# Performance work log

Measured on AMD Instinct MI355X. Metric: run time of the kernel, lower is better.

The kernel has to match this reference:

```python
import jax, jax.numpy as jnp
import numpy as np

B, S, Lc = 128, 128, 20          # batch, words per sentence, chars per word
AB, E = 100, 64                  # char alphabet, char embedding dim
Hc, H, OUT = 256, 512, 50        # char hidden, word hidden, n tags
PAD = 0                          # padding idx for words and chars


def _cell_params(key, din, h):
    k1, k2, k3, k4 = jax.random.split(key, 4)
    return (jax.random.normal(k1, (4 * h, din)) * 0.05,
            jax.random.normal(k2, (4 * h, h)) * 0.05,
            jax.random.normal(k3, (4 * h,)) * 0.05,
            jax.random.normal(k4, (4 * h,)) * 0.05)


def setup_inputs() -> dict:
    key = jax.random.key(0)
    ks = jax.random.split(key, 12)
    x = jax.random.randint(ks[0], (B, S, Lc), 0, AB)
    emb = jax.random.normal(ks[1], (AB, E)) * 0.05
    emb = emb.at[PAD].set(0.0)  # nn.Embedding padding_idx row is zero
    cW_ih, cW_hh, cb_ih, cb_hh = _cell_params(ks[2], E, Hc)
    fW_ih, fW_hh, fb_ih, fb_hh = _cell_params(ks[3], Hc, H)
    bW_ih, bW_hh, bb_ih, bb_hh = _cell_params(ks[4], Hc, H)
    W1 = jax.random.normal(ks[5], (256, 2 * H)) * 0.05
    b1 = jax.random.normal(ks[6], (256,)) * 0.05
    W2 = jax.random.normal(ks[7], (256, 256)) * 0.05
    b2 = jax.random.normal(ks[8], (256,)) * 0.05
    W3 = jax.random.normal(ks[9], (OUT, 256)) * 0.05
    b3 = jax.random.normal(ks[10], (OUT,)) * 0.05
    return dict(x=x, emb=emb,
                cW_ih=cW_ih, cW_hh=cW_hh, cb_ih=cb_ih, cb_hh=cb_hh,
                fW_ih=fW_ih, fW_hh=fW_hh, fb_ih=fb_ih, fb_hh=fb_hh,
                bW_ih=bW_ih, bW_hh=bW_hh, bb_ih=bb_ih, bb_hh=bb_hh,
                W1=W1, b1=b1, W2=W2, b2=b2, W3=W3, b3=b3)


def _lstm_cell(x_t, h, c, W_ih, W_hh, b_ih, b_hh):
    # PyTorch LSTMCell: gates ordered i, f, g, o
    g = x_t @ W_ih.T + b_ih + h @ W_hh.T + b_hh
    i, f, gg, o = jnp.split(g, 4, axis=-1)
    c = jax.nn.sigmoid(f) * c + jax.nn.sigmoid(i) * jnp.tanh(gg)
    h = jax.nn.sigmoid(o) * jnp.tanh(c)
    return h, c


def _char_acceptor(e_seq, lengths, W_ih, W_hh, b_ih, b_hh, hsize):
    # e_seq: [N, T, E]; returns last non-padded hidden state per row: [N, hsize]
    N, T, _ = e_seq.shape
    h0 = jnp.zeros((N, hsize), e_seq.dtype)

    def step(carry, inp):
        h, c, last = carry
        x_t, t = inp
        h, c = _lstm_cell(x_t, h, c, W_ih, W_hh, b_ih, b_hh)
        last = jnp.where((lengths > t)[:, None], h, last)
        return (h, c, last), None

    xs = (jnp.swapaxes(e_seq, 0, 1), jnp.arange(T))
    (_, _, last), _ = jax.lax.scan(step, (h0, h0, h0), xs)
    return last


def _lstm_transduce(seq_tbd, W_ih, W_hh, b_ih, b_hh, hsize):
    # seq_tbd: [T, B, D] -> all hidden states [T, B, hsize]
    Tb = seq_tbd.shape[1]
    h0 = jnp.zeros((Tb, hsize), seq_tbd.dtype)

    def step(carry, x_t):
        h, c = carry
        h, c = _lstm_cell(x_t, h, c, W_ih, W_hh, b_ih, b_hh)
        return (h, c), h

    _, hs = jax.lax.scan(step, (h0, h0), seq_tbd)
    return hs


def reference(x, emb,
              cW_ih, cW_hh, cb_ih, cb_hh,
              fW_ih, fW_hh, fb_ih, fb_hh,
              bW_ih, bW_hh, bb_ih, bb_hh,
              W1, b1, W2, b2, W3, b3):
    Bx, Sx, Lx = x.shape
    xf = x.reshape(Bx * Sx, Lx)                       # all words flattened
    e = emb[xf]                                       # [B*S, Lc, E]
    lengths = (xf != PAD).sum(axis=1)
    char_out = _char_acceptor(e, lengths, cW_ih, cW_hh, cb_ih, cb_hh, Hc)
    word_seq = char_out.reshape(Bx, Sx, Hc)           # [B, S, Hc]

    seq_tbd = jnp.swapaxes(word_seq, 0, 1)            # [S, B, Hc]
    hs_f = _lstm_transduce(seq_tbd, fW_ih, fW_hh, fb_ih, fb_hh, H)
    hs_b = _lstm_transduce(seq_tbd[::-1], bW_ih, bW_hh, bb_ih, bb_hh, H)[::-1]
    hs = jnp.concatenate([hs_f, hs_b], axis=-1)       # [S, B, 2H]
    hs = jnp.swapaxes(hs, 0, 1)                       # [B, S, 2H]

    h1 = jax.nn.relu(hs @ W1.T + b1)
    h2 = jax.nn.relu(h1 @ W2.T + b2)
    logits = h2 @ W3.T + b3                           # [B, S, OUT]
    return jax.nn.log_softmax(logits, axis=2)
```

## Files before the change

### kernel.cpp

```cpp
#include <hip/hip_runtime.h>
#include <hip/hip_bf16.h>
#include <math.h>

typedef __hip_bfloat16 bf16;
typedef __attribute__((ext_vector_type(8))) short bf16x8;
typedef __attribute__((ext_vector_type(4))) float f32x4;
typedef long i64t;

#define NW   16384
#define LC   20
#define EDIM 64
#define HC   256
#define HW   512
#define SEQ  128
#define NOUT 50
#define FPAD 16

#define LOG2E 1.4426950408889634f
__device__ __forceinline__ float fex2(float x) {
  float r; asm("v_exp_f32 %0, %1" : "=v"(r) : "v"(x)); return r;
}
__device__ __forceinline__ float frcp(float x) {
  float r; asm("v_rcp_f32 %0, %1" : "=v"(r) : "v"(x)); return r;
}
__device__ __forceinline__ float flog2(float x) {
  float r; asm("v_log_f32 %0, %1" : "=v"(r) : "v"(x)); return r;
}
__device__ __forceinline__ float fsig(float x) { return frcp(1.f + fex2(-LOG2E * x)); }
__device__ __forceinline__ float ftanh(float x) {
  return 1.f - 2.f * frcp(1.f + fex2(2.f * LOG2E * x));
}

__device__ __forceinline__ unsigned short f2bu(float f) {
  bf16 h = __float2bfloat16(f);
  return *reinterpret_cast<unsigned short*>(&h);
}
__device__ __forceinline__ bf16x8 ld8(const unsigned short* p) {
  return *reinterpret_cast<const bf16x8*>(p);
}
__device__ __forceinline__ float fp8_to_f32(unsigned int b) {
  float r; asm("v_cvt_f32_fp8 %0, %1" : "=v"(r) : "v"(b)); return r;
}
__device__ __forceinline__ i64t ld8x(const unsigned char* p, bool f) {
  i64t r;
  if (f) asm volatile("global_load_dwordx2 %0, %1, off sc0" : "=v"(r) : "v"(p));
  else   asm volatile("global_load_dwordx2 %0, %1, off sc0 sc1" : "=v"(r) : "v"(p));
  return r;
}
__device__ __forceinline__ void st8x(unsigned char* p, i64t v, bool f) {
  if (f) asm volatile("global_store_dwordx2 %0, %1, off sc0" :: "v"(p), "v"(v) : "memory");
  else   asm volatile("global_store_dwordx2 %0, %1, off sc0 sc1" :: "v"(p), "v"(v) : "memory");
}
__device__ __forceinline__ int ldflagx(const int* p, bool f) {
  int r;
  if (f) asm volatile("global_load_dword %0, %1, off sc0" : "=v"(r) : "v"(p));
  else   asm volatile("global_load_dword %0, %1, off sc0 sc1" : "=v"(r) : "v"(p));
  return r;
}
__device__ __forceinline__ void stflagx(int* p, int v, bool f) {
  if (f) asm volatile("global_store_dword %0, %1, off sc0" :: "v"(p), "v"(v) : "memory");
  else   asm volatile("global_store_dword %0, %1, off sc0 sc1" :: "v"(p), "v"(v) : "memory");
}
#define MFMA(a, b, c)  __builtin_amdgcn_mfma_f32_16x16x32_bf16(a, b, c, 0, 0, 0)
#define MFMA8(a, b, c) __builtin_amdgcn_mfma_f32_16x16x32_fp8_fp8(a, b, c, 0, 0, 0)

__global__ __launch_bounds__(512, 1) void char_lstm(
    const int* __restrict__ x, const unsigned char* __restrict__ emb8,
    const unsigned char* __restrict__ Wc8, const float* __restrict__ bcT,
    unsigned short* __restrict__ lastT, const int* __restrict__ len) {
  __shared__ unsigned char Hs8[2][64][264];
  __shared__ _Float16 Cs[256][66];
  __shared__ int lenS[64];
  const int tid = threadIdx.x;
  const int w = tid >> 6, l = tid & 63;
  const int l16 = l & 15, lk8 = (l >> 4) * 8, q = l >> 4;
  const int w0 = blockIdx.x * 64;
  if (tid < 64) lenS[tid] = len[w0 + tid];

  for (int t = 0; t < LC; ++t) {
    const int cur = t & 1, nxt = cur ^ 1;
    int xi[4];
#pragma unroll
    for (int wh = 0; wh < 4; ++wh) xi[wh] = x[(w0 + wh * 16 + l16) * LC + t];
#pragma unroll
    for (int c = 0; c < 2; ++c) {
      const int chg = w * 2 + c;
      const int cc0 = chg * 64;
      f32x4 acc[4][4] = {};
#pragma unroll
      for (int kk = 0; kk < 2; ++kk) {
        const int k = kk * 32 + lk8;
        const unsigned char* wp = Wc8 + (size_t)(cc0 + l16) * 320 + k;
        i64t bv8[4];
#pragma unroll
        for (int g = 0; g < 4; ++g)
          bv8[g] = *reinterpret_cast<const i64t*>(wp + g * 16 * 320);
#pragma unroll
        for (int wh = 0; wh < 4; ++wh) {
          i64t a8 = *reinterpret_cast<const i64t*>(emb8 + (size_t)xi[wh] * 64 + k);
#pragma unroll
          for (int g = 0; g < 4; ++g) acc[wh][g] = MFMA8(bv8[g], a8, acc[wh][g]);
        }
      }
      if (t > 0) {
#pragma unroll
        for (int kk = 2; kk < 10; ++kk) {
          const int k = kk * 32 + lk8;
          const unsigned char* wp = Wc8 + (size_t)(cc0 + l16) * 320 + k;
          i64t bv8[4];
#pragma unroll
          for (int g = 0; g < 4; ++g)
            bv8[g] = *reinterpret_cast<const i64t*>(wp + g * 16 * 320);
#pragma unroll
          for (int wh = 0; wh < 4; ++wh) {
            i64t a8 = *reinterpret_cast<const i64t*>(&Hs8[cur][wh * 16 + l16][k - 64]);
#pragma unroll
            for (int g = 0; g < 4; ++g) acc[wh][g] = MFMA8(bv8[g], a8, acc[wh][g]);
          }
        }
      }
      float4 bb4[4];
#pragma unroll
      for (int e = 0; e < 4; ++e)
        bb4[e] = *reinterpret_cast<const float4*>(bcT + (chg * 16 + q * 4 + e) * 4);
      const int uoff = chg * 16 + q * 4;
#pragma unroll
      for (int wh = 0; wh < 4; ++wh) {
        const int wd = wh * 16 + l16;
        float hv[4];
#pragma unroll
        for (int e = 0; e < 4; ++e) {
          const int ug = chg * 16 + q * 4 + e;
          const float gi = acc[wh][0][e] + bb4[e].x;
          const float gf = acc[wh][1][e] + bb4[e].y;
          const float gg = acc[wh][2][e] + bb4[e].z;
          const float go = acc[wh][3][e] + bb4[e].w;
          const float cprev = t ? (float)Cs[ug][wd] : 0.f;
          const float ccv = fsig(gf) * cprev + fsig(gi) * ftanh(gg);
          Cs[ug][wd] = (_Float16)ccv;
          hv[e] = fsig(go) * ftanh(ccv);
        }
        const int d0 = __builtin_amdgcn_cvt_pk_fp8_f32(hv[0], hv[1], 0, false);
        const int d1 = __builtin_amdgcn_cvt_pk_fp8_f32(hv[2], hv[3], 0, false);
        const unsigned int pk = (unsigned int)(d0 & 0xFFFF) |
                                ((unsigned int)(d1 & 0xFFFF) << 16);
        *reinterpret_cast<unsigned int*>(&Hs8[nxt][wd][uoff]) = pk;
      }
    }
    __syncthreads();
    {
      const int wd = tid >> 3, sub = tid & 7;
      const int myl = lenS[wd];
      if (myl == t + 1 || (myl == 0 && t == 0)) {
        const int n = w0 + wd;
        const int lrow = ((n & 127) * 128 + (n >> 7)) * HC;
        if (myl == 0) {
          bf16x8 z = {};
#pragma unroll
          for (int j = 0; j < 4; ++j)
            *reinterpret_cast<bf16x8*>(lastT + lrow + sub * 32 + j * 8) = z;
        } else {
#pragma unroll
          for (int j = 0; j < 4; ++j) {
            unsigned int v0 = *reinterpret_cast<unsigned int*>(
                &Hs8[nxt][wd][sub * 32 + j * 8]);
            unsigned int v1 = *reinterpret_cast<unsigned int*>(
                &Hs8[nxt][wd][sub * 32 + j * 8 + 4]);
            union { unsigned short s[8]; bf16x8 v; } o;
#pragma unroll
            for (int b = 0; b < 4; ++b) {
              o.s[b]     = f2bu(fp8_to_f32((v0 >> (8 * b)) & 0xFF));
              o.s[4 + b] = f2bu(fp8_to_f32((v1 >> (8 * b)) & 0xFF));
            }
            *reinterpret_cast<bf16x8*>(lastT + lrow + sub * 32 + j * 8) = o.v;
          }
        }
      }
    }
  }
}

__global__ __launch_bounds__(512, 1) void word_lstm(
    const unsigned short* __restrict__ lastT,
    const unsigned short* __restrict__ W16,
    const unsigned short* __restrict__ W16b,
    const unsigned char* __restrict__ W8f,
    const unsigned char* __restrict__ W8b,
    const float* __restrict__ bfi, const float* __restrict__ bbi,
    unsigned char* __restrict__ hbL8,
    unsigned short* __restrict__ hsW,
    int* __restrict__ aflag) {
  const int bx = blockIdx.x;
  if ((bx & 7) > 1) return;
  __shared__ unsigned short Wlds16[64 * 256];
  __shared__ unsigned char  Wlds8[64 * 512];
  __shared__ unsigned short ht[128][24];
  __shared__ unsigned char  ht8[128][24];
  __shared__ int fastS;
  const int tid = threadIdx.x;
  const int w = tid >> 6, l = tid & 63;
  const int l16 = l & 15, lk8 = (l >> 4) * 8, q = l >> 4;
  const int dir = bx & 7;
  const int nb = bx >> 3;
  const int c0 = nb * 64;
  const unsigned short* Wx = dir ? W16b : W16;
  const unsigned char*  Wh = dir ? W8b : W8f;
  const float* bias = dir ? bbi : bfi;
  int* negcnt = aflag + (size_t)2 * SEQ * 32 * FPAD;
  if (tid == 0) {
    const int xcc = __builtin_amdgcn_s_getreg(20 | (31 << 11)) & 7;
    int* xc = negcnt + 16 + dir * 8 + xcc;
    __hip_atomic_fetch_add(xc, 1, __ATOMIC_RELAXED, __HIP_MEMORY_SCOPE_AGENT);
    __hip_atomic_fetch_add(negcnt, 1, __ATOMIC_RELAXED, __HIP_MEMORY_SCOPE_AGENT);
    while (__hip_atomic_load(negcnt, __ATOMIC_RELAXED, __HIP_MEMORY_SCOPE_AGENT) < 64)
      __builtin_amdgcn_s_sleep(2);
    fastS = (__hip_atomic_load(xc, __ATOMIC_RELAXED, __HIP_MEMORY_SCOPE_AGENT) == 32);
  }
  for (int ci = tid; ci < 64 * 32; ci += 512) {
    const int col = ci >> 5, kc = (ci & 31) * 8;
    const int kcs = kc ^ ((col & 15) * 8);
    *reinterpret_cast<bf16x8*>(&Wlds16[col * 256 + kcs]) =
        ld8(Wx + (size_t)(c0 + col) * 256 + kc);
  }
  for (int ci = tid; ci < 64 * 64; ci += 512) {
    const int col = ci >> 6, kb = (ci & 63) * 8;
    const int kbs = kb ^ ((col & 15) * 8);
    *reinterpret_cast<i64t*>(&Wlds8[col * 512 + kbs]) =
        *reinterpret_cast<const i64t*>(Wh + (size_t)(c0 + col) * 512 + kb);
  }
  const float b0 = bias[c0 + 0 * 16 + l16];
  const float b1 = bias[c0 + 1 * 16 + l16];
  const float b2 = bias[c0 + 2 * 16 + l16];
  const float b3 = bias[c0 + 3 * 16 + l16];
  const int ksw = l16 * 8;
  float cst[4];
#pragma unroll
  for (int i = 0; i < 4; ++i) cst[i] = 0.f;
  __syncthreads();
  const bool fast = (fastS != 0);
  const int bt = w * 16 + l16;

  for (int t = 0; t < SEQ; ++t) {
    const int cur = t & 1;
    const int pos = dir ? (SEQ - 1 - t) : t;
    f32x4 acc[4] = {};
#pragma unroll
    for (int kk = 0; kk < 8; ++kk) {
      const int k = kk * 32 + lk8;
      bf16x8 a0 = ld8(lastT + ((size_t)pos * 128 + bt) * HC + k);
      const int ks = k ^ ksw;
#pragma unroll
      for (int nn = 0; nn < 4; ++nn) {
        bf16x8 bv = ld8(&Wlds16[(l16 + nn * 16) * 256 + ks]);
        acc[nn] = MFMA(a0, bv, acc[nn]);
      }
    }
    if (t > 0) {
      if (w == 0) {
        const int* fp = aflag + (size_t)(dir * SEQ + (t - 1)) * 32 * FPAD;
        for (;;) {
          int v = 1;
          if (l < 32) v = ldflagx(fp + l * FPAD, fast);
          if (__ballot(v != 0) == ~0ull) break;
          __builtin_amdgcn_s_sleep(1);
        }
      }
      __syncthreads();
      i64t af8[16];
      const unsigned char* hp =
          hbL8 + (size_t)(((cur ^ 1) * 2 + dir) * 32) * 128 * 16;
#pragma unroll
      for (int kk = 0; kk < 16; ++kk) {
        const int u = kk * 32 + lk8;
        const int nbs = u >> 4, ul = u & 15;
        af8[kk] = ld8x(hp + ((size_t)nbs * 128 + bt) * 16 + ul, fast);
      }
      asm volatile("s_waitcnt vmcnt(0)" ::: "memory");
      __builtin_amdgcn_sched_barrier(0);
#pragma unroll
      for (int kk = 0; kk < 16; ++kk) {
        const int ks8 = (kk * 32 + lk8) ^ ksw;
#pragma unroll
        for (int nn = 0; nn < 4; ++nn) {
          i64t w8 = *reinterpret_cast<const i64t*>(
              &Wlds8[(l16 + nn * 16) * 512 + ks8]);
          acc[nn] = MFMA8(af8[kk], w8, acc[nn]);
        }
      }
    }
    float hvf[4];
    int bats[4];
#pragma unroll
    for (int e = 0; e < 4; ++e) {
      const float gi = acc[0][e] + b0;
      const float gf = acc[1][e] + b1;
      const float gg = acc[2][e] + b2;
      const float go = acc[3][e] + b3;
      const float ccv = fsig(gf) * cst[e] + fsig(gi) * ftanh(gg);
      cst[e] = ccv;
      const float hv = fsig(go) * ftanh(ccv);
      const int bat = w * 16 + q * 4 + e;
      ht[bat][l16] = f2bu(hv);
      hvf[e] = hv; bats[e] = bat;
    }
    {
      const int d0 = __builtin_amdgcn_cvt_pk_fp8_f32(hvf[0], hvf[1], 0, false);
      const int d1 = __builtin_amdgcn_cvt_pk_fp8_f32(hvf[2], hvf[3], 0, false);
      ht8[bats[0]][l16] = (unsigned char)(d0 & 255);
      ht8[bats[1]][l16] = (unsigned char)((d0 >> 8) & 255);
      ht8[bats[2]][l16] = (unsigned char)(d1 & 255);
      ht8[bats[3]][l16] = (unsigned char)((d1 >> 8) & 255);
    }
    __syncthreads();
    if (tid < 256) {
      const int ub = tid >> 1, uh = tid & 1;
      i64t hv8 = *reinterpret_cast<const i64t*>(&ht8[ub][uh * 8]);
      st8x(hbL8 + (size_t)((cur * 2 + dir) * 32 + nb) * 128 * 16
               + ub * 16 + uh * 8, hv8, fast);
    }
    if (t < SEQ - 1) {
      asm volatile("s_waitcnt vmcnt(0)" ::: "memory");
      __syncthreads();
      if (tid == 0)
        stflagx(aflag + ((size_t)(dir * SEQ + t) * 32 + nb) * FPAD, 1, fast);
    }
    if (tid < 256) {
      const int ub = tid >> 1, uh = tid & 1;
      bf16x8 hv = ld8(&ht[ub][uh * 8]);
      *reinterpret_cast<bf16x8*>(
          hsW + (((size_t)(dir * 32 + nb) * 128 + pos) * 128 + ub) * 16 + uh * 8) = hv;
    }
  }
}

__global__ __launch_bounds__(256) void mlp1_gemm(
    const unsigned short* __restrict__ hsW, const unsigned short* __restrict__ W1b,
    const float* __restrict__ bias, unsigned short* __restrict__ out) {
  const int tid = threadIdx.x;
  const int w = tid >> 6, l = tid & 63;
  const int l16 = l & 15, lk8 = (l >> 4) * 8;
  const int by = blockIdx.y;
  const int row0 = by * 128 + w * 32;
  const int col0 = blockIdx.x * 64;
  f32x4 acc[2][4] = {};
  for (int kk = 0; kk < 32; ++kk) {
    const int k = kk * 32 + lk8;
    const int dirk = k >> 9, u = k & 511, nbs = u >> 4, ul = u & 15;
    const int p0 = w * 32 + l16, p1 = p0 + 16;
    bf16x8 a0 = ld8(hsW + (((size_t)(dirk * 32 + nbs) * 128 + p0) * 128 + by) * 16 + ul);
    bf16x8 a1 = ld8(hsW + (((size_t)(dirk * 32 + nbs) * 128 + p1) * 128 + by) * 16 + ul);
    const unsigned short* wp = W1b + (size_t)(col0 + l16) * 1024 + k;
#pragma unroll
    for (int nn = 0; nn < 4; ++nn) {
      bf16x8 bv = ld8(wp + nn * 16 * 1024);
      acc[0][nn] = MFMA(a0, bv, acc[0][nn]);
      acc[1][nn] = MFMA(a1, bv, acc[1][nn]);
    }
  }
  const int cr = (l >> 4) * 4;
#pragma unroll
  for (int m = 0; m < 2; ++m)
#pragma unroll
    for (int nn = 0; nn < 4; ++nn)
#pragma unroll
      for (int e = 0; e < 4; ++e) {
        const int r = row0 + m * 16 + cr + e;
        const int c = col0 + nn * 16 + l16;
        out[(size_t)r * 256 + c] = f2bu(fmaxf(acc[m][nn][e] + bias[c], 0.f));
      }
}

__global__ __launch_bounds__(256) void mlp_gemm(
    const unsigned short* __restrict__ A, int lda,
    const unsigned short* __restrict__ W, int ldw,
    const float* __restrict__ bias, unsigned short* __restrict__ out,
    int ldo, int nk, int relu) {
  const int tid = threadIdx.x;
  const int w = tid >> 6, l = tid & 63;
  const int l16 = l & 15, lk8 = (l >> 4) * 8;
  const int row0 = blockIdx.y * 128 + w * 32;
  const int col0 = blockIdx.x * 64;
  f32x4 acc[2][4] = {};
  for (int kk = 0; kk < nk; ++kk) {
    const int k = kk * 32 + lk8;
    bf16x8 a0 = ld8(A + (size_t)(row0 + l16) * lda + k);
    bf16x8 a1 = ld8(A + (size_t)(row0 + 16 + l16) * lda + k);
    const unsigned short* wp = W + (size_t)(col0 + l16) * ldw + k;
    bf16x8 bb[4];
#pragma unroll
    for (int nn = 0; nn < 4; ++nn) bb[nn] = ld8(wp + nn * 16 * ldw);
#pragma unroll
    for (int nn = 0; nn < 4; ++nn) {
      acc[0][nn] = MFMA(a0, bb[nn], acc[0][nn]);
      acc[1][nn] = MFMA(a1, bb[nn], acc[1][nn]);
    }
  }
  const int cr = (l >> 4) * 4;
#pragma unroll
  for (int m = 0; m < 2; ++m)
#pragma unroll
    for (int nn = 0; nn < 4; ++nn)
#pragma unroll
      for (int e = 0; e < 4; ++e) {
        const int r = row0 + m * 16 + cr + e;
        const int c = col0 + nn * 16 + l16;
        float v = acc[m][nn][e] + bias[c];
        if (relu) v = fmaxf(v, 0.f);
        out[(size_t)r * ldo + c] = f2bu(v);
      }
}

__global__ __launch_bounds__(256) void logits_fused(
    const unsigned short* __restrict__ h2, const unsigned short* __restrict__ W3p,
    const float* __restrict__ b3, float* __restrict__ out) {
  __shared__ float gt[128][68];
  __shared__ float lseb[128];
  const int tid = threadIdx.x;
  const int w = tid >> 6, l = tid & 63;
  const int l16 = l & 15, lk8 = (l >> 4) * 8;
  const int r0 = blockIdx.x * 128;
  const int rr0 = w * 32 + l16, rr1 = rr0 + 16;
  f32x4 acc[2][4] = {};
#pragma unroll
  for (int kk = 0; kk < 8; ++kk) {
    const int k = kk * 32 + lk8;
    bf16x8 a0 = ld8(h2 + (size_t)(r0 + rr0) * 256 + k);
    bf16x8 a1 = ld8(h2 + (size_t)(r0 + rr1) * 256 + k);
#pragma unroll
    for (int nn = 0; nn < 4; ++nn) {
      bf16x8 bv = ld8(W3p + (size_t)(nn * 16 + l16) * 256 + k);
      acc[0][nn] = MFMA(a0, bv, acc[0][nn]);
      acc[1][nn] = MFMA(a1, bv, acc[1][nn]);
    }
  }
  const int cr = (l >> 4) * 4;
#pragma unroll
  for (int m = 0; m < 2; ++m)
#pragma unroll
    for (int nn = 0; nn < 4; ++nn)
#pragma unroll
      for (int e = 0; e < 4; ++e) {
        const int col = nn * 16 + l16;
        gt[w * 32 + m * 16 + cr + e][col] =
            acc[m][nn][e] + (col < NOUT ? b3[col] : 0.f);
      }
  __syncthreads();
  if (tid < 128) {
    float mx = -INFINITY;
#pragma unroll
    for (int j = 0; j < NOUT; ++j) mx = fmaxf(mx, gt[tid][j]);
    float s = 0.f;
#pragma unroll
    for (int j = 0; j < NOUT; ++j) s += fex2(LOG2E * (gt[tid][j] - mx));
    lseb[tid] = flog2(s) * 0.6931471805599453f + mx;
  }
  __syncthreads();
  for (int idx = tid; idx < 128 * NOUT; idx += 256) {
    const int r = idx / NOUT, j = idx - r * NOUT;
    out[(size_t)(r0 + r) * NOUT + j] = gt[r][j] - lseb[r];
  }
}

__global__ void prep_wx(const float* __restrict__ ih, unsigned short* __restrict__ dst,
                        int HU, int KI) {
  const long tot = (long)HU * 4 * KI;
  for (long idx = (long)blockIdx.x * blockDim.x + threadIdx.x; idx < tot;
       idx += (long)gridDim.x * blockDim.x) {
    const int row = (int)(idx / KI), k = (int)(idx % KI);
    const int chunk = row >> 6, c = row & 63;
    const int g = c >> 4, u = chunk * 16 + (c & 15);
    dst[idx] = f2bu(ih[(size_t)(g * HU + u) * KI + k]);
  }
}

__global__ void prep_wc8(const float* __restrict__ ih, const float* __restrict__ hh,
                         unsigned char* __restrict__ dst, int HU, int KI, int KH) {
  const int K = KI + KH;
  const long tot = (long)HU * 4 * (K / 2);
  for (long p = (long)blockIdx.x * blockDim.x + threadIdx.x; p < tot;
       p += (long)gridDim.x * blockDim.x) {
    const int row = (int)(p / (K / 2)), kp = (int)(p % (K / 2)) * 2;
    const int chunk = row >> 6, c = row & 63;
    const int g = c >> 4, u = chunk * 16 + (c & 15);
    const float a = (kp < KI) ? ih[(size_t)(g * HU + u) * KI + kp]
                              : hh[(size_t)(g * HU + u) * KH + (kp - KI)];
    const float b = (kp + 1 < KI) ? ih[(size_t)(g * HU + u) * KI + kp + 1]
                                  : hh[(size_t)(g * HU + u) * KH + (kp + 1 - KI)];
    const int d = __builtin_amdgcn_cvt_pk_fp8_f32(a, b, 0, false);
    *reinterpret_cast<unsigned short*>(dst + (size_t)row * K + kp) =
        (unsigned short)(d & 0xFFFF);
  }
}

__global__ void prep_w8(const float* __restrict__ hh, unsigned char* __restrict__ dst,
                        int HU, int KH) {
  const long tot = (long)HU * 4 * (KH / 2);
  for (long p = (long)blockIdx.x * blockDim.x + threadIdx.x; p < tot;
       p += (long)gridDim.x * blockDim.x) {
    const int row = (int)(p / (KH / 2)), kp = (int)(p % (KH / 2)) * 2;
    const int chunk = row >> 6, c = row & 63;
    const int g = c >> 4, u = chunk * 16 + (c & 15);
    const float a = hh[(size_t)(g * HU + u) * KH + kp];
    const float b = hh[(size_t)(g * HU + u) * KH + kp + 1];
    const int d = __builtin_amdgcn_cvt_pk_fp8_f32(a, b, 0, false);
    *reinterpret_cast<unsigned short*>(dst + (size_t)row * KH + kp) =
        (unsigned short)(d & 0xFFFF);
  }
}

__global__ void prep_bias(const float* bih, const float* bhh, float* dst, int HU) {
  const int idx = blockIdx.x * blockDim.x + threadIdx.x;
  if (idx < 4 * HU) {
    const int chunk = idx >> 6, c = idx & 63;
    const int g = c >> 4, u = chunk * 16 + (c & 15);
    dst[idx] = bih[g * HU + u] + bhh[g * HU + u];
  }
}

__global__ void prep_biasT(const float* bih, const float* bhh, float* dst, int HU) {
  const int idx = blockIdx.x * blockDim.x + threadIdx.x;
  if (idx < 4 * HU) {
    const int u = idx >> 2, g = idx & 3;
    dst[idx] = bih[g * HU + u] + bhh[g * HU + u];
  }
}

__global__ void conv_bf(const float* __restrict__ src, unsigned short* __restrict__ dst,
                        long n) {
  for (long i = (long)blockIdx.x * blockDim.x + threadIdx.x; i < n;
       i += (long)gridDim.x * blockDim.x)
    dst[i] = f2bu(src[i]);
}

__global__ void conv_fp8(const float* __restrict__ src, unsigned char* __restrict__ dst,
                         long n2) {
  for (long i = (long)blockIdx.x * blockDim.x + threadIdx.x; i < n2;
       i += (long)gridDim.x * blockDim.x) {
    const int d = __builtin_amdgcn_cvt_pk_fp8_f32(src[i * 2], src[i * 2 + 1], 0, false);
    *reinterpret_cast<unsigned short*>(dst + i * 2) = (unsigned short)(d & 0xFFFF);
  }
}

__global__ void prep_w3(const float* __restrict__ W3, unsigned short* __restrict__ dst) {
  const int i = blockIdx.x * blockDim.x + threadIdx.x;
  if (i < 64 * 256) {
    const int r = i >> 8;
    dst[i] = (r < NOUT) ? f2bu(W3[i]) : 0;
  }
}

__global__ void lengths_k(const int* x, int* len) {
  const int n = blockIdx.x * blockDim.x + threadIdx.x;
  if (n < NW) {
    int c = 0;
#pragma unroll
    for (int l = 0; l < LC; ++l) c += (x[(size_t)n * LC + l] != 0) ? 1 : 0;
    len[n] = c;
  }
}

__global__ void zero_k(int* p, int n) {
  const int i = blockIdx.x * blockDim.x + threadIdx.x;
  if (i < n) p[i] = 0;
}

__global__ void sentinel_k(float* out, int n) {
  const int i = blockIdx.x * blockDim.x + threadIdx.x;
  if (i < n) out[i] = 1000.0f;
}

extern "C" void kernel_launch(void* const* d_in, const int* in_sizes, int n_in,
                              void* d_out, int out_size, void* d_ws, size_t ws_size,
                              hipStream_t stream) {
  const int*   x     = (const int*)d_in[0];
  const float* emb   = (const float*)d_in[1];
  const float* cW_ih = (const float*)d_in[2];
  const float* cW_hh = (const float*)d_in[3];
  const float* cb_ih = (const float*)d_in[4];
  const float* cb_hh = (const float*)d_in[5];
  const float* fW_ih = (const float*)d_in[6];
  const float* fW_hh = (const float*)d_in[7];
  const float* fb_ih = (const float*)d_in[8];
  const float* fb_hh = (const float*)d_in[9];
  const float* bW_ih = (const float*)d_in[10];
  const float* bW_hh = (const float*)d_in[11];
  const float* bb_ih = (const float*)d_in[12];
  const float* bb_hh = (const float*)d_in[13];
  const float* W1 = (const float*)d_in[14];
  const float* b1 = (const float*)d_in[15];
  const float* W2 = (const float*)d_in[16];
  const float* b2 = (const float*)d_in[17];
  const float* W3 = (const float*)d_in[18];
  const float* b3 = (const float*)d_in[19];
  float* out = (float*)d_out;
  (void)in_sizes; (void)n_in;

  char* ws = (char*)d_ws;
  size_t off = 0;
  auto alloc = [&](size_t bytes) -> char* {
    char* p = ws + off;
    off += (bytes + 255) & ~(size_t)255;
    return p;
  };
  const int NFLAG = 2 * SEQ * 32 * FPAD + 32;
  int*            len_  = (int*)alloc((size_t)NW * 4);
  int*            aflag = (int*)alloc((size_t)NFLAG * 4);
  unsigned char*  emb8  = (unsigned char*)alloc((size_t)100 * EDIM);
  unsigned char*  Wc8   = (unsigned char*)alloc((size_t)1024 * 320);
  unsigned short* Wf_i  = (unsigned short*)alloc((size_t)2048 * 256 * 2);
  unsigned short* Wb_i  = (unsigned short*)alloc((size_t)2048 * 256 * 2);
  unsigned char*  Wf8   = (unsigned char*)alloc((size_t)2048 * 512);
  unsigned char*  Wb8   = (unsigned char*)alloc((size_t)2048 * 512);
  unsigned short* W1b   = (unsigned short*)alloc((size_t)256 * 1024 * 2);
  unsigned short* W2b   = (unsigned short*)alloc((size_t)256 * 256 * 2);
  unsigned short* W3p   = (unsigned short*)alloc((size_t)64 * 256 * 2);
  float*          bcT   = (float*)alloc(1024 * 4);
  float*          bf_i  = (float*)alloc(2048 * 4);
  float*          bb_i  = (float*)alloc(2048 * 4);
  unsigned short* lastT = (unsigned short*)alloc((size_t)NW * HC * 2);
  unsigned char*  hbL8  = (unsigned char*)alloc((size_t)2 * 2 * 32 * 128 * 16);
  unsigned short* hsW   = (unsigned short*)alloc((size_t)2 * 32 * 128 * 128 * 16 * 2);
  unsigned short* h1    = (unsigned short*)alloc((size_t)NW * HC * 2);
  unsigned short* h2    = (unsigned short*)alloc((size_t)NW * HC * 2);

  if (off > ws_size) {
    sentinel_k<<<(out_size + 255) / 256, 256, 0, stream>>>(out, out_size);
    return;
  }

  auto cdiv = [](long a, long b) { return (int)((a + b - 1) / b); };

  prep_wc8<<<640, 256, 0, stream>>>(cW_ih, cW_hh, Wc8, HC, EDIM, HC);
  prep_wx<<<1024, 256, 0, stream>>>(fW_ih, Wf_i, HW, HC);
  prep_wx<<<1024, 256, 0, stream>>>(bW_ih, Wb_i, HW, HC);
  prep_w8<<<2048, 256, 0, stream>>>(fW_hh, Wf8, HW, HW);
  prep_w8<<<2048, 256, 0, stream>>>(bW_hh, Wb8, HW, HW);
  prep_biasT<<<cdiv(1024, 256), 256, 0, stream>>>(cb_ih, cb_hh, bcT, HC);
  prep_bias<<<cdiv(2048, 256), 256, 0, stream>>>(fb_ih, fb_hh, bf_i, HW);
  prep_bias<<<cdiv(2048, 256), 256, 0, stream>>>(bb_ih, bb_hh, bb_i, HW);
  conv_fp8<<<13, 256, 0, stream>>>(emb, emb8, 100L * EDIM / 2);
  conv_bf<<<1024, 256, 0, stream>>>(W1, W1b, 256L * 1024);
  conv_bf<<<256, 256, 0, stream>>>(W2, W2b, 256L * 256);
  prep_w3<<<64, 256, 0, stream>>>(W3, W3p);
  lengths_k<<<cdiv(NW, 256), 256, 0, stream>>>(x, len_);
  zero_k<<<cdiv(NFLAG, 256), 256, 0, stream>>>(aflag, NFLAG);

  char_lstm<<<NW / 64, 512, 0, stream>>>(x, emb8, Wc8, bcT, lastT, len_);

  word_lstm<<<256, 512, 0, stream>>>(lastT, Wf_i, Wb_i, Wf8, Wb8, bf_i, bb_i,
                                     hbL8, hsW, aflag);

  mlp1_gemm<<<dim3(4, 128), 256, 0, stream>>>(hsW, W1b, b1, h1);
  mlp_gemm<<<dim3(4, 128), 256, 0, stream>>>(h1, 256, W2b, 256, b2, h2, 256, 8, 1);
  logits_fused<<<NW / 128, 256, 0, stream>>>(h2, W3p, b3, out);
}
```

Baseline: 1.126 ms.

## Store word hidden states in FP8 and run MLP1 with FP8 MFMA

The word LSTM now writes each step's hidden state straight to the global exchange buffer as single bytes, without staging through LDS first. This drops one barrier and the bf16 copy of the hidden state. The per-position hidden-state history is stored in FP8 instead of bf16, and W1 is converted to FP8 so the first MLP layer uses the fp8 MFMA. This cuts memory traffic and shortens the serial step's critical path, at the cost of lower precision in the first MLP layer and many small byte stores.

```diff
diff --git a/kernel.cpp b/kernel.cpp
--- a/kernel.cpp
+++ b/kernel.cpp
@@ -47,9 +47,9 @@
   else   asm volatile("global_load_dwordx2 %0, %1, off sc0 sc1" : "=v"(r) : "v"(p));
   return r;
 }
-__device__ __forceinline__ void st8x(unsigned char* p, i64t v, bool f) {
-  if (f) asm volatile("global_store_dwordx2 %0, %1, off sc0" :: "v"(p), "v"(v) : "memory");
-  else   asm volatile("global_store_dwordx2 %0, %1, off sc0 sc1" :: "v"(p), "v"(v) : "memory");
+__device__ __forceinline__ void stbx(unsigned char* p, unsigned int v, bool f) {
+  if (f) asm volatile("global_store_byte %0, %1, off sc0" :: "v"(p), "v"(v) : "memory");
+  else   asm volatile("global_store_byte %0, %1, off sc0 sc1" :: "v"(p), "v"(v) : "memory");
 }
 __device__ __forceinline__ int ldflagx(const int* p, bool f) {
   int r;
@@ -188,13 +188,12 @@
     const unsigned char* __restrict__ W8b,
     const float* __restrict__ bfi, const float* __restrict__ bbi,
     unsigned char* __restrict__ hbL8,
-    unsigned short* __restrict__ hsW,
+    unsigned char* __restrict__ hs8,
     int* __restrict__ aflag) {
   const int bx = blockIdx.x;
   if ((bx & 7) > 1) return;
   __shared__ unsigned short Wlds16[64 * 256];
   __shared__ unsigned char  Wlds8[64 * 512];
-  __shared__ unsigned short ht[128][24];
   __shared__ unsigned char  ht8[128][24];
   __shared__ int fastS;
   const int tid = threadIdx.x;
@@ -288,8 +287,7 @@
         }
       }
     }
-    float hvf[4];
-    int bats[4];
+    unsigned char* hb = hbL8 + (size_t)((cur * 2 + dir) * 32 + nb) * 128 * 16;
 #pragma unroll
     for (int e = 0; e < 4; ++e) {
       const float gi = acc[0][e] + b0;
@@ -299,42 +297,26 @@
       const float ccv = fsig(gf) * cst[e] + fsig(gi) * ftanh(gg);
       cst[e] = ccv;
       const float hv = fsig(go) * ftanh(ccv);
+      const int d = __builtin_amdgcn_cvt_pk_fp8_f32(hv, hv, 0, false);
       const int bat = w * 16 + q * 4 + e;
-      ht[bat][l16] = f2bu(hv);
-      hvf[e] = hv; bats[e] = bat;
-    }
-    {
-      const int d0 = __builtin_amdgcn_cvt_pk_fp8_f32(hvf[0], hvf[1], 0, false);
-      const int d1 = __builtin_amdgcn_cvt_pk_fp8_f32(hvf[2], hvf[3], 0, false);
-      ht8[bats[0]][l16] = (unsigned char)(d0 & 255);
-      ht8[bats[1]][l16] = (unsigned char)((d0 >> 8) & 255);
-      ht8[bats[2]][l16] = (unsigned char)(d1 & 255);
-      ht8[bats[3]][l16] = (unsigned char)((d1 >> 8) & 255);
-    }
+      ht8[bat][l16] = (unsigned char)(d & 255);
+      stbx(hb + bat * 16 + l16, (unsigned int)(d & 255), fast);
+    }
+    asm volatile("s_waitcnt vmcnt(0)" ::: "memory");
     __syncthreads();
+    if (t < SEQ - 1 && tid == 0)
+      stflagx(aflag + ((size_t)(dir * SEQ + t) * 32 + nb) * FPAD, 1, fast);
     if (tid < 256) {
       const int ub = tid >> 1, uh = tid & 1;
       i64t hv8 = *reinterpret_cast<const i64t*>(&ht8[ub][uh * 8]);
-      st8x(hbL8 + (size_t)((cur * 2 + dir) * 32 + nb) * 128 * 16
-               + ub * 16 + uh * 8, hv8, fast);
-    }
-    if (t < SEQ - 1) {
-      asm volatile("s_waitcnt vmcnt(0)" ::: "memory");
-      __syncthreads();
-      if (tid == 0)
-        stflagx(aflag + ((size_t)(dir * SEQ + t) * 32 + nb) * FPAD, 1, fast);
-    }
-    if (tid < 256) {
-      const int ub = tid >> 1, uh = tid & 1;
-      bf16x8 hv = ld8(&ht[ub][uh * 8]);
-      *reinterpret_cast<bf16x8*>(
-          hsW + (((size_t)(dir * 32 + nb) * 128 + pos) * 128 + ub) * 16 + uh * 8) = hv;
+      *reinterpret_cast<i64t*>(
+          hs8 + (((size_t)(dir * 32 + nb) * 128 + pos) * 128 + ub) * 16 + uh * 8) = hv8;
     }
   }
 }
 
 __global__ __launch_bounds__(256) void mlp1_gemm(
-    const unsigned short* __restrict__ hsW, const unsigned short* __restrict__ W1b,
+    const unsigned char* __restrict__ hs8, const unsigned char* __restrict__ W18,
     const float* __restrict__ bias, unsigned short* __restrict__ out) {
   const int tid = threadIdx.x;
   const int w = tid >> 6, l = tid & 63;
@@ -347,14 +329,16 @@
     const int k = kk * 32 + lk8;
     const int dirk = k >> 9, u = k & 511, nbs = u >> 4, ul = u & 15;
     const int p0 = w * 32 + l16, p1 = p0 + 16;
-    bf16x8 a0 = ld8(hsW + (((size_t)(dirk * 32 + nbs) * 128 + p0) * 128 + by) * 16 + ul);
-    bf16x8 a1 = ld8(hsW + (((size_t)(dirk * 32 + nbs) * 128 + p1) * 128 + by) * 16 + ul);
-    const unsigned short* wp = W1b + (size_t)(col0 + l16) * 1024 + k;
+    i64t a0 = *reinterpret_cast<const i64t*>(
+        hs8 + (((size_t)(dirk * 32 + nbs) * 128 + p0) * 128 + by) * 16 + ul);
+    i64t a1 = *reinterpret_cast<const i64t*>(
+        hs8 + (((size_t)(dirk * 32 + nbs) * 128 + p1) * 128 + by) * 16 + ul);
+    const unsigned char* wp = W18 + (size_t)(col0 + l16) * 1024 + k;
 #pragma unroll
     for (int nn = 0; nn < 4; ++nn) {
-      bf16x8 bv = ld8(wp + nn * 16 * 1024);
-      acc[0][nn] = MFMA(a0, bv, acc[0][nn]);
-      acc[1][nn] = MFMA(a1, bv, acc[1][nn]);
+      i64t bv = *reinterpret_cast<const i64t*>(wp + nn * 16 * 1024);
+      acc[0][nn] = MFMA8(a0, bv, acc[0][nn]);
+      acc[1][nn] = MFMA8(a1, bv, acc[1][nn]);
     }
   }
   const int cr = (l >> 4) * 4;
@@ -611,7 +595,7 @@
   unsigned short* Wb_i  = (unsigned short*)alloc((size_t)2048 * 256 * 2);
   unsigned char*  Wf8   = (unsigned char*)alloc((size_t)2048 * 512);
   unsigned char*  Wb8   = (unsigned char*)alloc((size_t)2048 * 512);
-  unsigned short* W1b   = (unsigned short*)alloc((size_t)256 * 1024 * 2);
+  unsigned char*  W18   = (unsigned char*)alloc((size_t)256 * 1024);
   unsigned short* W2b   = (unsigned short*)alloc((size_t)256 * 256 * 2);
   unsigned short* W3p   = (unsigned short*)alloc((size_t)64 * 256 * 2);
   float*          bcT   = (float*)alloc(1024 * 4);
@@ -619,7 +603,7 @@
   float*          bb_i  = (float*)alloc(2048 * 4);
   unsigned short* lastT = (unsigned short*)alloc((size_t)NW * HC * 2);
   unsigned char*  hbL8  = (unsigned char*)alloc((size_t)2 * 2 * 32 * 128 * 16);
-  unsigned short* hsW   = (unsigned short*)alloc((size_t)2 * 32 * 128 * 128 * 16 * 2);
+  unsigned char*  hs8   = (unsigned char*)alloc((size_t)2 * 32 * 128 * 128 * 16);
   unsigned short* h1    = (unsigned short*)alloc((size_t)NW * HC * 2);
   unsigned short* h2    = (unsigned short*)alloc((size_t)NW * HC * 2);
 
@@ -639,7 +623,7 @@
   prep_bias<<<cdiv(2048, 256), 256, 0, stream>>>(fb_ih, fb_hh, bf_i, HW);
   prep_bias<<<cdiv(2048, 256), 256, 0, stream>>>(bb_ih, bb_hh, bb_i, HW);
   conv_fp8<<<13, 256, 0, stream>>>(emb, emb8, 100L * EDIM / 2);
-  conv_bf<<<1024, 256, 0, stream>>>(W1, W1b, 256L * 1024);
+  conv_fp8<<<512, 256, 0, stream>>>(W1, W18, 256L * 1024 / 2);
   conv_bf<<<256, 256, 0, stream>>>(W2, W2b, 256L * 256);
   prep_w3<<<64, 256, 0, stream>>>(W3, W3p);
   lengths_k<<<cdiv(NW, 256), 256, 0, stream>>>(x, len_);
@@ -648,9 +632,9 @@
   char_lstm<<<NW / 64, 512, 0, stream>>>(x, emb8, Wc8, bcT, lastT, len_);
 
   word_lstm<<<256, 512, 0, stream>>>(lastT, Wf_i, Wb_i, Wf8, Wb8, bf_i, bb_i,
-                                     hbL8, hsW, aflag);
-
-  mlp1_gemm<<<dim3(4, 128), 256, 0, stream>>>(hsW, W1b, b1, h1);
+                                     hbL8, hs8, aflag);
+
+  mlp1_gemm<<<dim3(4, 128), 256, 0, stream>>>(hs8, W18, b1, h1);
   mlp_gemm<<<dim3(4, 128), 256, 0, stream>>>(h1, 256, W2b, 256, b2, h2, 256, 8, 1);
   logits_fused<<<NW / 128, 256, 0, stream>>>(h2, W3p, b3, out);
 }
```

Result: no change. 1.127 ms (+0.1%).
